# Kernel tuning notes

Hardware: AMD Instinct MI355X
Metric: run time of the kernel (lower is better)

The kernel has to match this reference:

```python
import jax, jax.numpy as jnp
import numpy as np

DIM = 256
NUM_HEADS = 8
HEAD_DIM = DIM // NUM_HEADS
CPB_HIDDEN = 512
B, N = 2, 2304
TABLE = 9025  # (2*48-1)**2


def _l2norm(t, eps=1e-12):
    # matches torch F.normalize(dim=-1): x / max(||x||, eps)
    n = jnp.sqrt(jnp.sum(t * t, axis=-1, keepdims=True))
    return t / jnp.maximum(n, eps)


def setup_inputs() -> dict:
    key = jax.random.key(0)
    ks = jax.random.split(key, 12)
    x = jax.random.normal(ks[0], (B, N, DIM), dtype=jnp.float32)
    relative_pos_index = jax.random.randint(ks[1], (N, N), 0, TABLE, dtype=jnp.int64)
    relative_coords_table = jax.random.uniform(ks[2], (TABLE, 2), dtype=jnp.float32) * 2.0 - 1.0
    seq_length_scale = jnp.ones((1,), dtype=jnp.float32) * jnp.log2(jnp.float32(N))
    padding_mask = jnp.zeros((B, N), dtype=jnp.int32)
    s = 0.02
    W_qkv = jax.random.normal(ks[3], (3 * DIM, DIM), dtype=jnp.float32) * s
    b_qkv = jnp.zeros((3 * DIM,), dtype=jnp.float32)
    # temperature init: log(exp(1/0.24) - 1) so softplus(temperature) = 1/0.24
    temperature = jnp.full((NUM_HEADS, 1, 1), float(np.log(np.expm1(1.0 / 0.24))), dtype=jnp.float32)
    query_embedding = jax.random.normal(ks[4], (NUM_HEADS, 1, HEAD_DIM), dtype=jnp.float32) * s
    W_proj = jax.random.normal(ks[5], (DIM, DIM), dtype=jnp.float32) * s
    b_proj = jnp.zeros((DIM,), dtype=jnp.float32)
    W_cpb1 = jax.random.normal(ks[6], (CPB_HIDDEN, 2), dtype=jnp.float32) * s
    b_cpb1 = jnp.zeros((CPB_HIDDEN,), dtype=jnp.float32)
    W_cpb2 = jax.random.normal(ks[7], (NUM_HEADS, CPB_HIDDEN), dtype=jnp.float32) * s
    b_cpb2 = jnp.zeros((NUM_HEADS,), dtype=jnp.float32)
    return {
        'x': x, 'relative_pos_index': relative_pos_index,
        'relative_coords_table': relative_coords_table,
        'seq_length_scale': seq_length_scale, 'padding_mask': padding_mask,
        'W_qkv': W_qkv, 'b_qkv': b_qkv, 'temperature': temperature,
        'query_embedding': query_embedding, 'W_proj': W_proj, 'b_proj': b_proj,
        'W_cpb1': W_cpb1, 'b_cpb1': b_cpb1, 'W_cpb2': W_cpb2, 'b_cpb2': b_cpb2,
    }


def reference(x, relative_pos_index, relative_coords_table, seq_length_scale,
              padding_mask, W_qkv, b_qkv, temperature, query_embedding,
              W_proj, b_proj, W_cpb1, b_cpb1, W_cpb2, b_cpb2):
    Bx, Nx, C = x.shape
    h, d = NUM_HEADS, HEAD_DIM
    # qkv projection -> (B, 3h, N, d); first h heads = q, then k, then v
    qkv = (jnp.einsum('bnc,oc->bno', x, W_qkv) + b_qkv)
    qkv = qkv.reshape(Bx, Nx, 3 * h, d).transpose(0, 2, 1, 3)
    q, k, v = qkv[:, :h], qkv[:, h:2 * h], qkv[:, 2 * h:]
    # CPB relative bias: (T,2) -> (T,h) -> (h,N,N) via gather
    hid = jax.nn.relu(relative_coords_table @ W_cpb1.T + b_cpb1)
    tab = hid @ W_cpb2.T + b_cpb2                    # (T, h)
    rel_bias = tab.T[:, relative_pos_index.reshape(-1)].reshape(h, Nx, Nx)
    # cosine-sim attention with learned query embedding + softplus temperature
    scale = jax.nn.softplus(temperature) * seq_length_scale[0]   # (h,1,1)
    qn = (_l2norm(q) + query_embedding) * scale                  # (B,h,N,d)
    kn = _l2norm(k)
    attn = jnp.einsum('bhnd,bhmd->bhnm', qn, kn) + rel_bias
    attn = jax.nn.softmax(attn, axis=-1)
    out = jnp.einsum('bhnm,bhmd->bhnd', attn, v)
    out = out.transpose(0, 2, 1, 3).reshape(Bx, Nx, C)
    out = out @ W_proj.T + b_proj
    return out
```

## Files before the change

kernel.cpp:

```cpp
#include <hip/hip_runtime.h>
#include <math.h>

#define DIMC 256
#define NHEADS 8
#define HDIM 32
#define CPBH 512
#define BB 2
#define NSEQ 2304
#define TAB 9025
#define TABP 9040
#define RTOT (BB*NHEADS*NSEQ)
#define SPLITS 4
#define MSP (NSEQ/SPLITS)
#define PBS 34
#define NCHUNK (NSEQ/32)
#define LOG2E 1.44269504088896340736f

#define IDXP_ELEMS    (NSEQ * NCHUNK * 16)
#define IDXP4_BLOCKS  (IDXP_ELEMS / 1024)
#define CPB_BLOCKS    ((TAB + 63) / 64)
#define QKV_BLOCKS    (12 * 72)

typedef unsigned short ushort;
typedef __attribute__((ext_vector_type(8))) short short8;
typedef __attribute__((ext_vector_type(4))) short short4v;
typedef __attribute__((ext_vector_type(4))) float f32x4;

#define MFMA16(a,b,c) __builtin_amdgcn_mfma_f32_16x16x32_bf16((a),(b),(c),0,0,0)

#define GL16(SRC, DST) __builtin_amdgcn_global_load_lds( \
    (const __attribute__((address_space(1))) void*)(SRC), \
    (__attribute__((address_space(3))) void*)(DST), 16, 0, 0)

__device__ __forceinline__ ushort f2bf(float x) {
  unsigned u = __float_as_uint(x);
  u += 0x7FFFu + ((u >> 16) & 1u);
  return (ushort)(u >> 16);
}
__device__ __forceinline__ float bf2f(ushort b) {
  return __uint_as_float(((unsigned)b) << 16);
}
__device__ __forceinline__ float fexp2(float x) {
#if defined(__has_builtin)
#if __has_builtin(__builtin_amdgcn_exp2f)
  return __builtin_amdgcn_exp2f(x);
#else
  return exp2f(x);
#endif
#else
  return exp2f(x);
#endif
}
__device__ __forceinline__ unsigned pack_trunc(float p0, float p1) {
  return __builtin_amdgcn_perm(__float_as_uint(p1), __float_as_uint(p0), 0x07060302u);
}
__device__ __forceinline__ void cvt8(const float* __restrict__ p, short8* hi, short8* lo) {
  float4 v0 = *(const float4*)p;
  float4 v1 = *(const float4*)(p + 4);
  float vv[8] = {v0.x, v0.y, v0.z, v0.w, v1.x, v1.y, v1.z, v1.w};
  short8 h, l;
#pragma unroll
  for (int i = 0; i < 8; ++i) {
    ushort hh = f2bf(vv[i]);
    h[i] = (short)hh;
    l[i] = (short)f2bf(vv[i] - bf2f(hh));
  }
  *hi = h; *lo = l;
}

__launch_bounds__(256)
__global__ void pack_kernel(const int* __restrict__ idx, unsigned* __restrict__ idxP) {
  int t4 = blockIdx.x * 256 + threadIdx.x;
  int grp = t4 >> 4;
  int ch = grp % NCHUNK;
  int n4 = grp / NCHUNK;
  int m = ch * 32 + (t4 & 15);
  unsigned o[4];
#pragma unroll
  for (int i = 0; i < 4; ++i) {
    unsigned lo = (unsigned)idx[(size_t)(n4 * 4 + i) * NSEQ + m];
    unsigned hi = (unsigned)idx[(size_t)(n4 * 4 + i) * NSEQ + m + 16];
    o[i] = lo | (hi << 16);
  }
  *(uint4*)&idxP[(size_t)t4 * 4] = *(const uint4*)o;
}

__launch_bounds__(256)
__global__ void pre_kernel(const float* __restrict__ x, const float* __restrict__ wq,
                           const float* __restrict__ tbl, const float* __restrict__ W1,
                           const float* __restrict__ b1, const float* __restrict__ W2,
                           const float* __restrict__ b2,
                           const float* __restrict__ bias, const float* __restrict__ temp,
                           const float* __restrict__ sls, const float* __restrict__ qe,
                           ushort* __restrict__ qhi, ushort* __restrict__ qlo,
                           ushort* __restrict__ khi, ushort* __restrict__ klo,
                           ushort* __restrict__ vT, ushort* __restrict__ tabBf) {
  __shared__ __align__(16) ushort smemu[33792];
  int blk = blockIdx.x;
  int tid = threadIdx.x;

  if (blk < CPB_BLOCKS) {
    float* smem = (float*)smemu;
    float* w1b = smem;
    float* w2t = smem + 2048;
    float* part = smem + 6144;
    for (int i = tid; i < CPBH; i += 256) {
      w1b[i * 4 + 0] = W1[2 * i];
      w1b[i * 4 + 1] = W1[2 * i + 1];
      w1b[i * 4 + 2] = b1[i];
      w1b[i * 4 + 3] = 0.f;
    }
    for (int i = tid; i < CPBH * NHEADS; i += 256)
      w2t[(i & (CPBH - 1)) * NHEADS + (i >> 9)] = W2[i];
    int tl = tid & 63, jc = tid >> 6;
    int t = blk * 64 + tl;
    bool valid = t < TAB;
    float c0 = 0.f, c1 = 0.f;
    if (valid) { c0 = tbl[2 * t]; c1 = tbl[2 * t + 1]; }
    __syncthreads();
    float acc[NHEADS];
#pragma unroll
    for (int h = 0; h < NHEADS; ++h) acc[h] = 0.f;
    for (int j = jc * 128; j < jc * 128 + 128; ++j) {
      float4 wv = *(const float4*)&w1b[j * 4];
      float hid = fmaxf(fmaf(c0, wv.x, fmaf(c1, wv.y, wv.z)), 0.f);
      float4 wa = *(const float4*)&w2t[j * NHEADS];
      float4 wb = *(const float4*)&w2t[j * NHEADS + 4];
      acc[0] = fmaf(hid, wa.x, acc[0]);
      acc[1] = fmaf(hid, wa.y, acc[1]);
      acc[2] = fmaf(hid, wa.z, acc[2]);
      acc[3] = fmaf(hid, wa.w, acc[3]);
      acc[4] = fmaf(hid, wb.x, acc[4]);
      acc[5] = fmaf(hid, wb.y, acc[5]);
      acc[6] = fmaf(hid, wb.z, acc[6]);
      acc[7] = fmaf(hid, wb.w, acc[7]);
    }
#pragma unroll
    for (int h = 0; h < NHEADS; ++h) part[((size_t)jc * 64 + tl) * NHEADS + h] = acc[h];
    __syncthreads();
    if (jc == 0 && valid) {
#pragma unroll
      for (int h = 0; h < NHEADS; ++h) {
        float s = b2[h];
#pragma unroll
        for (int p = 0; p < 4; ++p) s += part[((size_t)p * 64 + tl) * NHEADS + h];
        tabBf[h * TABP + t] = f2bf(s * LOG2E);
      }
    }
  } else {
    ushort* bsh = smemu;
    ushort* bsl = smemu + 64 * 264;
    float (*vbuf)[65] = (float(*)[65])smemu;
    int t = blk - CPB_BLOCKS;
    int n0 = (t % 12) * 64, m0 = (t / 12) * 64;
    int lane = tid & 63, w = tid >> 6;
    int g = lane >> 4, c = lane & 15;
    int mw = m0 + w * 16;
    const int K = DIMC;

    {
      int rr = tid >> 2, cq = (tid & 3) * 64;
#pragma unroll
      for (int j = 0; j < 64; j += 8) {
        short8 hh, ll;
        cvt8(&wq[(size_t)(n0 + rr) * K + cq + j], &hh, &ll);
        *(short8*)&bsh[rr * 264 + cq + j] = hh;
        *(short8*)&bsl[rr * 264 + cq + j] = ll;
      }
    }
    __syncthreads();

    f32x4 acc[4] = {{0,0,0,0},{0,0,0,0},{0,0,0,0},{0,0,0,0}};
#pragma unroll 2
    for (int k0 = 0; k0 < K; k0 += 32) {
      short8 ah, al;
      cvt8(&x[(size_t)(mw + c) * K + k0 + g * 8], &ah, &al);
#pragma unroll
      for (int nt = 0; nt < 4; ++nt) {
        int br = (nt * 16 + c) * 264 + k0 + g * 8;
        short8 bh = *(const short8*)&bsh[br];
        short8 bl = *(const short8*)&bsl[br];
        acc[nt] = MFMA16(ah, bh, acc[nt]);
        acc[nt] = MFMA16(al, bh, acc[nt]);
        acc[nt] = MFMA16(ah, bl, acc[nt]);
      }
    }
#pragma unroll
    for (int nt = 0; nt < 4; ++nt) {
      float bv = bias[n0 + nt * 16 + c];
#pragma unroll
      for (int r = 0; r < 4; ++r) acc[nt][r] += bv;
    }
    __syncthreads();

    int b = (m0 >= NSEQ) ? 1 : 0;
    int nb = m0 - b * NSEQ;
    int sect = n0 >> 8;
    int hloc = (n0 & 255) >> 5;

    if (sect < 2) {
#pragma unroll
      for (int H = 0; H < 2; ++H) {
        int head = hloc + H;
        float scale = (sect == 0) ? log1pf(expf(temp[head])) * sls[0] * LOG2E : 0.f;
#pragma unroll
        for (int r = 0; r < 4; ++r) {
          float ss = acc[2*H][r]*acc[2*H][r] + acc[2*H+1][r]*acc[2*H+1][r];
          ss += __shfl_xor(ss, 1);
          ss += __shfl_xor(ss, 2);
          ss += __shfl_xor(ss, 4);
          ss += __shfl_xor(ss, 8);
          float inv = 1.f / fmaxf(sqrtf(ss), 1e-12f);
#pragma unroll
          for (int half = 0; half < 2; ++half) {
            int d = half * 16 + c;
            float val = acc[2*H + half][r] * inv;
            if (sect == 0) val = (val + qe[head * HDIM + d]) * scale;
            vbuf[w * 16 + g * 4 + r][H * 32 + d] = val;
          }
        }
      }
      __syncthreads();
      int plane = tid >> 7;
      int seg = tid & 127;
      int head = seg >> 6, row = seg & 63;
      const float* srcrow = &vbuf[row][head * 32];
      ushort out16[32];
#pragma unroll
      for (int i = 0; i < 32; ++i) {
        float v = srcrow[i];
        ushort hh = f2bf(v);
        out16[i] = plane ? f2bf(v - bf2f(hh)) : hh;
      }
      ushort* dstp = plane ? (sect == 0 ? qlo : klo) : (sect == 0 ? qhi : khi);
      size_t off = ((size_t)(b * NHEADS + hloc + head) * NSEQ + nb + row) * HDIM;
#pragma unroll
      for (int q4 = 0; q4 < 4; ++q4)
        *(int4*)&dstp[off + q4 * 8] = ((int4*)out16)[q4];
    } else {
#pragma unroll
      for (int nt = 0; nt < 4; ++nt)
#pragma unroll
        for (int r = 0; r < 4; ++r)
          vbuf[w * 16 + g * 4 + r][nt * 16 + c] = acc[nt][r];
      __syncthreads();
      int hbase = (n0 - 512) >> 5;
#pragma unroll
      for (int it = 0; it < 16; ++it) {
        int dloc = (tid >> 6) * 16 + it;
        int p = tid & 63;
        int pp = p & 31;
        int nsrc = (p & 32) + (pp & 1) * 16 + (pp >> 1);
        float v = vbuf[nsrc][dloc];
        int head = hbase + (dloc >> 5), d = dloc & 31;
        vT[((size_t)((b * NHEADS + head) * HDIM + d)) * NSEQ + nb + p] = f2bf(v);
      }
    }
  }
}

__launch_bounds__(256)
__global__ void attn_kernel(const ushort* __restrict__ qhi, const ushort* __restrict__ qlo,
                            const ushort* __restrict__ khi, const ushort* __restrict__ klo,
                            const ushort* __restrict__ vT, const ushort* __restrict__ tabBf,
                            const unsigned* __restrict__ idxP,
                            float* __restrict__ pO, float* __restrict__ pL) {
  __shared__ ushort tbf[9216];
  __shared__ __align__(16) ushort pbuf[8][16 * PBS];
  __shared__ __align__(16) ushort stg[2][6144];
  int tid = threadIdx.x;
  int lane = tid & 63;
  int w = tid >> 6;

  int bid = blockIdx.x;
  int qb = bid >> 5;
  int k8 = bid & 7;
  int j4 = (bid >> 3) & 3;
  int y  = k8 + 8 * j4;
  int s = y & 3, h = y >> 2;

  const ushort* tsrc = tabBf + h * TABP;
#pragma unroll
  for (int i = 0; i < 4; ++i) {
    int off = i * 2048 + tid * 8;
    *(int4*)&tbf[off] = *(const int4*)&tsrc[off];
  }
  if (tid < 128) {
    int off = 8192 + tid * 8;
    *(int4*)&tbf[off] = *(const int4*)&tsrc[off];
  }

  int g = lane >> 4, c = lane & 15;
  int q0 = qb * 64 + w * 16;
  int qg0 = q0 >> 2;
  size_t rowA = (size_t)h * NSEQ;
  size_t rowB = (size_t)(NHEADS + h) * NSEQ;
  int m0 = s * MSP;

  int su   = tid & 127;
  int srow = su & 31;
  int sslt = su >> 5;
  const ushort* kb0 = (tid < 128) ? khi : klo;
  const ushort* sA = kb0 + (rowA + m0 + srow) * HDIM + sslt * 8;
  const ushort* sB = kb0 + (rowB + m0 + srow) * HDIM + sslt * 8;
  const ushort* sV = vT + ((size_t)(((tid < 128) ? h : NHEADS + h) * HDIM + srow)) * NSEQ
                     + m0 + sslt * 8;
  unsigned dwb = (unsigned)(tid & 192) * 8;

#define STAGE(DP) do {                         \
    GL16(sA, (DP) + dwb);                      \
    GL16(sB, (DP) + 2048 + dwb);               \
    GL16(sV, (DP) + 4096 + dwb);               \
    sA += 32 * HDIM; sB += 32 * HDIM; sV += 32; \
  } while (0)

  short8 qAh = *(const short8*)&qhi[(rowA + q0 + c) * HDIM + g * 8];
  short8 qAl = *(const short8*)&qlo[(rowA + q0 + c) * HDIM + g * 8];
  short8 qBh = *(const short8*)&qhi[(rowB + q0 + c) * HDIM + g * 8];
  short8 qBl = *(const short8*)&qlo[(rowB + q0 + c) * HDIM + g * 8];

  unsigned oIb = (unsigned)(((unsigned)(qg0 + g) * NCHUNK + (m0 >> 5)) * 64 + c * 4);
  unsigned oI  = oIb;
  uint4 ia = *(const uint4*)&idxP[oI];

  STAGE(&stg[0][0]);
  __syncthreads();

  short one = (c == 0) ? (short)0x3F80 : (short)0;
  short8 onesB = {one, one, one, one, one, one, one, one};

  f32x4 oa0 = {0,0,0,0}, oa1 = {0,0,0,0}, ob0 = {0,0,0,0}, ob1 = {0,0,0,0};
  f32x4 la = {0,0,0,0}, lb = {0,0,0,0};
  ushort* pba = pbuf[w * 2];
  ushort* pbb = pbuf[w * 2 + 1];

  int kbo = g * 256 + c * 8;
  int cur = 0;

  for (int mt = m0; mt < m0 + MSP; mt += 32) {
    bool lastit = (mt + 32 >= m0 + MSP);
    unsigned oIn = lastit ? oIb : oI + 64;
    uint4 ian = *(const uint4*)&idxP[oIn];
    oI = oIn;
    if (!lastit) STAGE(&stg[cur ^ 1][0]);

    const ushort* S = &stg[cur][0];
    short8 ak0h = *(const short8*)&S[kbo];
    short8 ak1h = *(const short8*)&S[kbo + 128];
    short8 ak0l = *(const short8*)&S[1024 + kbo];
    short8 ak1l = *(const short8*)&S[1024 + kbo + 128];
    short8 bk0h = *(const short8*)&S[2048 + kbo];
    short8 bk1h = *(const short8*)&S[2048 + kbo + 128];
    short8 bk0l = *(const short8*)&S[3072 + kbo];
    short8 bk1l = *(const short8*)&S[3072 + kbo + 128];

    f32x4 sa0 = {0,0,0,0}, sa1 = {0,0,0,0}, sb0 = {0,0,0,0}, sb1 = {0,0,0,0};
    sa0 = MFMA16(qAh, ak0h, sa0);
    sa1 = MFMA16(qAh, ak1h, sa1);
    sb0 = MFMA16(qBh, bk0h, sb0);
    sb1 = MFMA16(qBh, bk1h, sb1);
    sa0 = MFMA16(qAl, ak0h, sa0);
    sa1 = MFMA16(qAl, ak1h, sa1);
    sb0 = MFMA16(qBl, bk0h, sb0);
    sb1 = MFMA16(qBl, bk1h, sb1);
    sa0 = MFMA16(qAh, ak0l, sa0);
    sa1 = MFMA16(qAh, ak1l, sa1);
    sb0 = MFMA16(qBh, bk0l, sb0);
    sb1 = MFMA16(qBh, bk1l, sb1);

    unsigned ip[4] = {ia.x, ia.y, ia.z, ia.w};
    float b0[4], b1[4];
#pragma unroll
    for (int r = 0; r < 4; ++r) {
      b0[r] = bf2f(tbf[ip[r] & 0xFFFF]);
      b1[r] = bf2f(tbf[ip[r] >> 16]);
    }
#pragma unroll
    for (int r = 0; r < 4; ++r) {
      float pA0 = fexp2(sa0[r] + b0[r]);
      float pA1 = fexp2(sa1[r] + b1[r]);
      *(unsigned*)&pba[(g * 4 + r) * PBS + 2 * c] = pack_trunc(pA0, pA1);
      float pB0 = fexp2(sb0[r] + b0[r]);
      float pB1 = fexp2(sb1[r] + b1[r]);
      *(unsigned*)&pbb[(g * 4 + r) * PBS + 2 * c] = pack_trunc(pB0, pB1);
    }

    short4v paA = *(const short4v*)&pba[c * PBS + g * 8];
    short4v paB = *(const short4v*)&pba[c * PBS + g * 8 + 4];
    short8 pfa = __builtin_shufflevector(paA, paB, 0, 1, 2, 3, 4, 5, 6, 7);
    short4v pbA = *(const short4v*)&pbb[c * PBS + g * 8];
    short4v pbB = *(const short4v*)&pbb[c * PBS + g * 8 + 4];
    short8 pfb = __builtin_shufflevector(pbA, pbB, 0, 1, 2, 3, 4, 5, 6, 7);

    short8 vf0 = *(const short8*)&S[4096 + kbo];
    short8 vf1 = *(const short8*)&S[4096 + kbo + 128];
    short8 wf0 = *(const short8*)&S[5120 + kbo];
    short8 wf1 = *(const short8*)&S[5120 + kbo + 128];

    oa0 = MFMA16(pfa, vf0, oa0);
    oa1 = MFMA16(pfa, vf1, oa1);
    ob0 = MFMA16(pfb, wf0, ob0);
    ob1 = MFMA16(pfb, wf1, ob1);
    la  = MFMA16(pfa, onesB, la);
    lb  = MFMA16(pfb, onesB, lb);

    ia = ian;
    __syncthreads();
    cur ^= 1;
  }
#undef STAGE

  size_t prowA = (size_t)s * RTOT + rowA;
  size_t prowB = (size_t)s * RTOT + rowB;
#pragma unroll
  for (int r = 0; r < 4; ++r) {
    size_t pra = prowA + q0 + g * 4 + r;
    pO[pra * HDIM + c]      = oa0[r];
    pO[pra * HDIM + 16 + c] = oa1[r];
    size_t prb = prowB + q0 + g * 4 + r;
    pO[prb * HDIM + c]      = ob0[r];
    pO[prb * HDIM + 16 + c] = ob1[r];
    if (c == 0) { pL[pra] = la[r]; pL[prb] = lb[r]; }
  }
}

#define ALD 264
__launch_bounds__(256)
__global__ void gemm_proj_fused(const float* __restrict__ pO, const float* __restrict__ pL,
                                const float* __restrict__ Wp,
                                const float* __restrict__ bias, float* __restrict__ C) {
  __shared__ __align__(16) ushort Ahs[32 * ALD];
  __shared__ __align__(16) ushort Als[32 * ALD];
  int tid = threadIdx.x;
  int m0 = blockIdx.x * 32;
  int b = (m0 >= NSEQ) ? 1 : 0;
  int nb = m0 - b * NSEQ;

  {
    int rr = tid >> 3;
    int q  = tid & 3;
    int hp = (tid >> 2) & 1;
    int n = nb + rr;
#pragma unroll
    for (int hh = 0; hh < 4; ++hh) {
      int h = hp * 4 + hh;
      size_t bhn = (size_t)(b * NHEADS + h) * NSEQ + n;
      float L = 0.f;
#pragma unroll
      for (int sp = 0; sp < SPLITS; ++sp) L += pL[(size_t)sp * RTOT + bhn];
      float inv = 1.f / L;
      float a[8] = {0.f, 0.f, 0.f, 0.f, 0.f, 0.f, 0.f, 0.f};
#pragma unroll
      for (int sp = 0; sp < SPLITS; ++sp) {
        const float* src = &pO[((size_t)sp * RTOT + bhn) * HDIM + q * 8];
        float4 v0 = *(const float4*)&src[0];
        float4 v1 = *(const float4*)&src[4];
        a[0] += v0.x; a[1] += v0.y; a[2] += v0.z; a[3] += v0.w;
        a[4] += v1.x; a[5] += v1.y; a[6] += v1.z; a[7] += v1.w;
      }
      ushort hi8[8], lo8[8];
#pragma unroll
      for (int i = 0; i < 8; ++i) {
        float v = a[i] * inv;
        ushort hh2 = f2bf(v);
        hi8[i] = hh2;
        lo8[i] = f2bf(v - bf2f(hh2));
      }
      int k = h * 32 + q * 8;
      *(int4*)&Ahs[rr * ALD + k] = *(int4*)hi8;
      *(int4*)&Als[rr * ALD + k] = *(int4*)lo8;
    }
  }
  __syncthreads();

  int lane = tid & 63, w = tid >> 6;
  int g = lane >> 4, c = lane & 15;
  int n0 = w * 64;
  f32x4 acc[2][4] = {};
  for (int k0 = 0; k0 < DIMC; k0 += 32) {
    short8 bfh[4], bfl[4];
#pragma unroll
    for (int nt = 0; nt < 4; ++nt)
      cvt8(&Wp[(size_t)(n0 + nt * 16 + c) * DIMC + k0 + g * 8], &bfh[nt], &bfl[nt]);
#pragma unroll
    for (int mt = 0; mt < 2; ++mt) {
      short8 ah = *(const short8*)&Ahs[(mt * 16 + c) * ALD + k0 + g * 8];
      short8 al = *(const short8*)&Als[(mt * 16 + c) * ALD + k0 + g * 8];
#pragma unroll
      for (int nt = 0; nt < 4; ++nt) {
        acc[mt][nt] = MFMA16(ah, bfh[nt], acc[mt][nt]);
        acc[mt][nt] = MFMA16(al, bfh[nt], acc[mt][nt]);
        acc[mt][nt] = MFMA16(ah, bfl[nt], acc[mt][nt]);
      }
    }
  }
#pragma unroll
  for (int nt = 0; nt < 4; ++nt) {
    float bv = bias[n0 + nt * 16 + c];
#pragma unroll
    for (int mt = 0; mt < 2; ++mt)
#pragma unroll
      for (int r = 0; r < 4; ++r)
        C[(size_t)(m0 + mt * 16 + g * 4 + r) * DIMC + n0 + nt * 16 + c] = acc[mt][nt][r] + bv;
  }
}

extern "C" void kernel_launch(void* const* d_in, const int* in_sizes, int n_in,
                              void* d_out, int out_size, void* d_ws, size_t ws_size,
                              hipStream_t stream) {
  const float* x    = (const float*)d_in[0];
  const int*   idx  = (const int*)d_in[1];
  const float* tbl  = (const float*)d_in[2];
  const float* sls  = (const float*)d_in[3];
  const float* Wqkv = (const float*)d_in[5];
  const float* bqkv = (const float*)d_in[6];
  const float* temp = (const float*)d_in[7];
  const float* qe   = (const float*)d_in[8];
  const float* Wp   = (const float*)d_in[9];
  const float* bp   = (const float*)d_in[10];
  const float* W1   = (const float*)d_in[11];
  const float* b1   = (const float*)d_in[12];
  const float* W2   = (const float*)d_in[13];
  const float* b2   = (const float*)d_in[14];

  float* ws   = (float*)d_ws;
  float* pO   = ws;
  float* pL   = pO + (size_t)SPLITS * RTOT * HDIM;
  unsigned* idxP = (unsigned*)(pL + (size_t)SPLITS * RTOT);
  ushort* u   = (ushort*)(idxP + IDXP_ELEMS);
  ushort* qhi = u;                u += (size_t)RTOT * HDIM;
  ushort* qlo = u;                u += (size_t)RTOT * HDIM;
  ushort* khi = u;                u += (size_t)RTOT * HDIM;
  ushort* klo = u;                u += (size_t)RTOT * HDIM;
  ushort* vT  = u;                u += (size_t)RTOT * HDIM;
  ushort* tabBf = u;              u += 73728;
  float* out  = (float*)d_out;

  pack_kernel<<<dim3(IDXP4_BLOCKS), dim3(256), 0, stream>>>(idx, idxP);
  pre_kernel<<<dim3(CPB_BLOCKS + QKV_BLOCKS), dim3(256), 0, stream>>>(
      x, Wqkv, tbl, W1, b1, W2, b2, bqkv, temp, sls, qe,
      qhi, qlo, khi, klo, vT, tabBf);
  attn_kernel<<<dim3((NSEQ / 64) * NHEADS * SPLITS), dim3(256), 0, stream>>>(
      qhi, qlo, khi, klo, vT, tabBf, idxP, pO, pL);
  gemm_proj_fused<<<dim3((BB * NSEQ) / 32), dim3(256), 0, stream>>>(
      pO, pL, Wp, bp, out);
}
```

Baseline: 223.0 us.

## Deepen K/V staging pipeline to four LDS buffers with one barrier per tile

```diff
diff --git a/kernel.cpp b/kernel.cpp
--- a/kernel.cpp
+++ b/kernel.cpp
@@ -12,6 +12,7 @@
 #define RTOT (BB*NHEADS*NSEQ)
 #define SPLITS 4
 #define MSP (NSEQ/SPLITS)
+#define NT (MSP/32)
 #define PBS 34
 #define NCHUNK (NSEQ/32)
 #define LOG2E 1.44269504088896340736f
@@ -267,7 +268,7 @@
                             float* __restrict__ pO, float* __restrict__ pL) {
   __shared__ ushort tbf[9216];
   __shared__ __align__(16) ushort pbuf[8][16 * PBS];
-  __shared__ __align__(16) ushort stg[2][6144];
+  __shared__ __align__(16) ushort stg[4][6144];
   int tid = threadIdx.x;
   int lane = tid & 63;
   int w = tid >> 6;
@@ -301,17 +302,17 @@
   int srow = su & 31;
   int sslt = su >> 5;
   const ushort* kb0 = (tid < 128) ? khi : klo;
-  const ushort* sA = kb0 + (rowA + m0 + srow) * HDIM + sslt * 8;
-  const ushort* sB = kb0 + (rowB + m0 + srow) * HDIM + sslt * 8;
-  const ushort* sV = vT + ((size_t)(((tid < 128) ? h : NHEADS + h) * HDIM + srow)) * NSEQ
-                     + m0 + sslt * 8;
+  const ushort* sA0 = kb0 + (rowA + m0 + srow) * HDIM + sslt * 8;
+  const ushort* sB0 = kb0 + (rowB + m0 + srow) * HDIM + sslt * 8;
+  const ushort* sV0 = vT + ((size_t)(((tid < 128) ? h : NHEADS + h) * HDIM + srow)) * NSEQ
+                      + m0 + sslt * 8;
   unsigned dwb = (unsigned)(tid & 192) * 8;
 
-#define STAGE(DP) do {                         \
-    GL16(sA, (DP) + dwb);                      \
-    GL16(sB, (DP) + 2048 + dwb);               \
-    GL16(sV, (DP) + 4096 + dwb);               \
-    sA += 32 * HDIM; sB += 32 * HDIM; sV += 32; \
+#define STAGE(BUF, TILE) do {                              \
+    ushort* d_ = &stg[(BUF)][0] + dwb;                     \
+    GL16(sA0 + (size_t)(TILE) * 32 * HDIM, d_);            \
+    GL16(sB0 + (size_t)(TILE) * 32 * HDIM, d_ + 2048);     \
+    GL16(sV0 + (TILE) * 32,                d_ + 4096);     \
   } while (0)
 
   short8 qAh = *(const short8*)&qhi[(rowA + q0 + c) * HDIM + g * 8];
@@ -320,10 +321,12 @@
   short8 qBl = *(const short8*)&qlo[(rowB + q0 + c) * HDIM + g * 8];
 
   unsigned oIb = (unsigned)(((unsigned)(qg0 + g) * NCHUNK + (m0 >> 5)) * 64 + c * 4);
-  unsigned oI  = oIb;
-  uint4 ia = *(const uint4*)&idxP[oI];
-
-  STAGE(&stg[0][0]);
+  uint4 ia0 = *(const uint4*)&idxP[oIb];
+  uint4 ia1 = *(const uint4*)&idxP[oIb + 64];
+
+  STAGE(0, 0);
+  STAGE(1, 1);
+  STAGE(2, 2);
   __syncthreads();
 
   short one = (c == 0) ? (short)0x3F80 : (short)0;
@@ -335,16 +338,18 @@
   ushort* pbb = pbuf[w * 2 + 1];
 
   int kbo = g * 256 + c * 8;
-  int cur = 0;
-
-  for (int mt = m0; mt < m0 + MSP; mt += 32) {
-    bool lastit = (mt + 32 >= m0 + MSP);
-    unsigned oIn = lastit ? oIb : oI + 64;
-    uint4 ian = *(const uint4*)&idxP[oIn];
-    oI = oIn;
-    if (!lastit) STAGE(&stg[cur ^ 1][0]);
-
-    const ushort* S = &stg[cur][0];
+
+  for (int t = 0; t < NT; ++t) {
+    asm volatile("s_waitcnt vmcnt(8)" ::: "memory");
+    __builtin_amdgcn_s_barrier();
+    __builtin_amdgcn_sched_barrier(0);
+
+    int t2 = t + 2; if (t2 >= NT) t2 -= NT;
+    int t3 = t + 3; if (t3 >= NT) t3 -= NT;
+    uint4 ian = *(const uint4*)&idxP[oIb + (unsigned)t2 * 64];
+    STAGE((t + 3) & 3, t3);
+
+    const ushort* S = &stg[t & 3][0];
     short8 ak0h = *(const short8*)&S[kbo];
     short8 ak1h = *(const short8*)&S[kbo + 128];
     short8 ak0l = *(const short8*)&S[1024 + kbo];
@@ -368,7 +373,7 @@
     sb0 = MFMA16(qBh, bk0l, sb0);
     sb1 = MFMA16(qBh, bk1l, sb1);
 
-    unsigned ip[4] = {ia.x, ia.y, ia.z, ia.w};
+    unsigned ip[4] = {ia0.x, ia0.y, ia0.z, ia0.w};
     float b0[4], b1[4];
 #pragma unroll
     for (int r = 0; r < 4; ++r) {
@@ -404,11 +409,11 @@
     la  = MFMA16(pfa, onesB, la);
     lb  = MFMA16(pfb, onesB, lb);
 
-    ia = ian;
-    __syncthreads();
-    cur ^= 1;
+    ia0 = ia1; ia1 = ian;
   }
 #undef STAGE
+
+  asm volatile("s_waitcnt vmcnt(0)" ::: "memory");
 
   size_t prowA = (size_t)s * RTOT + rowA;
   size_t prowB = (size_t)s * RTOT + rowB;
```

New measurement: 245.2 us. 1.1x slower.
